# Kernel optimization log

Hardware: AMD Instinct MI355X
Metric: run time of the kernel (lower is better)

## Reference

```python
import jax, jax.numpy as jnp
import numpy as np

SIG_T_TRAIN = 0.07
SIG_T_INFER = 0.07
EPS = 1e-12  # torch F.normalize eps


def _l2_normalize(x):
    # matches torch.nn.functional.normalize(x, dim=-1): x / max(||x||_2, eps)
    nrm = jnp.sqrt(jnp.sum(x * x, axis=-1, keepdims=True))
    return x / jnp.maximum(nrm, EPS)


def setup_inputs() -> dict:
    key = jax.random.key(0)
    k1, k2 = jax.random.split(key)
    v_feat = jax.random.normal(k1, (32, 16, 256, 512), dtype=jnp.float32)  # (b,n,t,d)
    t_feat = jax.random.normal(k2, (512, 512), dtype=jnp.float32)          # (c,d)
    return {"v_feat": v_feat, "t_feat": t_feat, "split": 1}


def reference(v_feat, t_feat, split):
    # split: 1 -> 'test' (normalize + sig_T_infer), 0 -> train (sig_T_train)
    if split == 1:
        tau = SIG_T_INFER
        v_feat = _l2_normalize(v_feat)
        t_feat = _l2_normalize(t_feat)
    else:
        tau = SIG_T_TRAIN
    # Original: dist = einsum('bntd,bmcd->bctnm', v, t_repeated)/tau, then mean over m, then n.
    # t_repeated is identical along m (a pure repeat), so mean over m is a no-op, and the
    # mean over n commutes with the linear contraction: reduce over n first, never
    # materializing the (b,c,t,n,m) tensor.
    v_mean = jnp.mean(v_feat, axis=1)  # (b,t,d)
    dist = jnp.einsum('btd,cd->bct', v_mean, t_feat) / tau  # (b,c,t)
    return dist
```

## Files before the change

kernel.cpp:

```cpp
#include <hip/hip_runtime.h>

typedef unsigned short u16;
typedef unsigned int u32;

typedef __bf16 bf16x8 __attribute__((ext_vector_type(8)));
typedef float f32x4 __attribute__((ext_vector_type(4)));

__device__ __forceinline__ u16 f2bf(float f) {
    u32 u = __float_as_uint(f);
    return (u16)((u + 0x7fffu + ((u >> 16) & 1u)) >> 16);
}

__global__ __launch_bounds__(256, 4) void prep_kernel(
    const float* __restrict__ v,
    const float* __restrict__ tf,
    u16* __restrict__ vm,
    u16* __restrict__ tn,
    const int* __restrict__ splitp)
{
    const int tid  = threadIdx.x;
    const int w    = tid >> 6;
    const int lane = tid & 63;
    const int g    = lane >> 4;
    const int l15  = lane & 15;
    const int split = *splitp;
    const int bxx  = blockIdx.x;

    if (bxx >= 8192) {
        const int row = (bxx - 8192) * 16 + w * 4 + g;
        const float* rp = tf + (size_t)row * 512;
        float4 x[8];
#pragma unroll
        for (int i = 0; i < 8; i++)
            x[i] = *reinterpret_cast<const float4*>(rp + i * 64 + l15 * 4);
        float s = 0.f;
#pragma unroll
        for (int i = 0; i < 8; i++)
            s += x[i].x*x[i].x + x[i].y*x[i].y + x[i].z*x[i].z + x[i].w*x[i].w;
#pragma unroll
        for (int off = 1; off < 16; off <<= 1) s += __shfl_xor(s, off, 64);
        float inv = 1.0f;
        if (split == 1) inv = 1.0f / fmaxf(sqrtf(s), 1e-12f);
        u16* orow = tn + (size_t)row * 512;
#pragma unroll
        for (int i = 0; i < 8; i++) {
            uint2 pk;
            pk.x = (u32)f2bf(x[i].x*inv) | ((u32)f2bf(x[i].y*inv) << 16);
            pk.y = (u32)f2bf(x[i].z*inv) | ((u32)f2bf(x[i].w*inv) << 16);
            *reinterpret_cast<uint2*>(orow + i * 64 + l15 * 4) = pk;
        }
        return;
    }

    const int b = bxx >> 8;
    const int t = bxx & 255;
    const int n = w * 4 + g;
    const float* rp = v + (((size_t)(b * 16 + n) * 256) + t) * 512;

    float4 x[8];
#pragma unroll
    for (int i = 0; i < 8; i++)
        x[i] = *reinterpret_cast<const float4*>(rp + i * 64 + l15 * 4);

    float s = 0.f;
#pragma unroll
    for (int i = 0; i < 8; i++)
        s += x[i].x*x[i].x + x[i].y*x[i].y + x[i].z*x[i].z + x[i].w*x[i].w;
#pragma unroll
    for (int off = 1; off < 16; off <<= 1) s += __shfl_xor(s, off, 64);
    float inv = 1.0f;
    if (split == 1) inv = 1.0f / fmaxf(sqrtf(s), 1e-12f);

#pragma unroll
    for (int i = 0; i < 8; i++) {
        x[i].x *= inv; x[i].y *= inv; x[i].z *= inv; x[i].w *= inv;
    }

#pragma unroll
    for (int off = 16; off < 64; off <<= 1)
#pragma unroll
        for (int i = 0; i < 8; i++) {
            x[i].x += __shfl_xor(x[i].x, off, 64);
            x[i].y += __shfl_xor(x[i].y, off, 64);
            x[i].z += __shfl_xor(x[i].z, off, 64);
            x[i].w += __shfl_xor(x[i].w, off, 64);
        }

    __shared__ float lds[4][512];
#pragma unroll
    for (int i = 0; i < 8; i++) {
        if ((i >> 1) == g)
            *reinterpret_cast<float4*>(&lds[w][i * 64 + l15 * 4]) = x[i];
    }
    __syncthreads();

    float2 r; r.x = 0.f; r.y = 0.f;
#pragma unroll
    for (int w2 = 0; w2 < 4; w2++) {
        float2 p = *reinterpret_cast<const float2*>(&lds[w2][tid * 2]);
        r.x += p.x; r.y += p.y;
    }
    r.x *= 0.0625f; r.y *= 0.0625f;
    u32 packed = (u32)f2bf(r.x) | ((u32)f2bf(r.y) << 16);
    reinterpret_cast<u32*>(vm)[((size_t)(b * 256 + t) << 8) + tid] = packed;
}

__global__ __launch_bounds__(256) void gemm_kernel(
    const u16* __restrict__ tn,
    const u16* __restrict__ vm,
    float* __restrict__ out)
{
    const int tid  = threadIdx.x;
    const int lane = tid & 63;
    const int wid  = tid >> 6;
    const int wm   = wid & 1;
    const int wn   = wid >> 1;
    const int quad = lane >> 4;
    const int l15  = lane & 15;

    const int c0 = blockIdx.x * 64 + wm * 32;
    const int t0 = blockIdx.y * 64 + wn * 32;
    const int b  = blockIdx.z;

    const u16* A0 = tn + (size_t)(c0 + l15) * 512 + quad * 8;
    const u16* B0 = vm + (size_t)b * 131072 + (size_t)(t0 + l15) * 512 + quad * 8;

    f32x4 acc[2][2] = {};
#pragma unroll 4
    for (int kk = 0; kk < 512; kk += 32) {
        bf16x8 af[2], bf[2];
#pragma unroll
        for (int i = 0; i < 2; i++)
            af[i] = *reinterpret_cast<const bf16x8*>(A0 + (size_t)i * 16 * 512 + kk);
#pragma unroll
        for (int j = 0; j < 2; j++)
            bf[j] = *reinterpret_cast<const bf16x8*>(B0 + (size_t)j * 16 * 512 + kk);
#pragma unroll
        for (int i = 0; i < 2; i++)
#pragma unroll
            for (int j = 0; j < 2; j++)
                acc[i][j] = __builtin_amdgcn_mfma_f32_16x16x32_bf16(
                    af[i], bf[j], acc[i][j], 0, 0, 0);
    }

    const float sc = 1.0f / 0.07f;
    float* ob = out + (size_t)b * 131072;
#pragma unroll
    for (int i = 0; i < 2; i++)
#pragma unroll
        for (int j = 0; j < 2; j++)
#pragma unroll
            for (int r = 0; r < 4; r++)
                ob[(c0 + i * 16 + quad * 4 + r) * 256 + (t0 + j * 16 + l15)]
                    = acc[i][j][r] * sc;
}

extern "C" void kernel_launch(void* const* d_in, const int* in_sizes, int n_in,
                              void* d_out, int out_size, void* d_ws, size_t ws_size,
                              hipStream_t stream) {
    const float* v_feat = (const float*)d_in[0];
    const float* t_feat = (const float*)d_in[1];
    const int*   splitp = (const int*)d_in[2];
    float* out = (float*)d_out;

    u16* tn = (u16*)d_ws;
    u16* vm = tn + 512 * 512;

    prep_kernel<<<dim3(8192 + 32), dim3(256), 0, stream>>>(v_feat, t_feat, vm, tn, splitp);
    gemm_kernel<<<dim3(8, 4, 32), dim3(256), 0, stream>>>(tn, vm, out);
}
```

Before: 389.4 us.

## Stage GEMM operands through padded LDS tiles with larger 128x64 block tile

The GEMM kernel now cooperatively loads 128x64 A and 64x64 B tiles into padded shared memory per 64-wide K step, and each wave reads its MFMA fragments from LDS instead of straight from global memory. The block tile grows from 64x64 to 128x64, so each wave computes 4x2 MFMA tiles and the grid halves in x. The aim is more operand reuse and fewer redundant global loads. The cost is extra barriers, LDS traffic and fewer blocks. The GEMM is small next to the memory-bound prep kernel, which reads 256MB, so the total effect is likely minor.

```diff
diff --git a/kernel.cpp b/kernel.cpp
--- a/kernel.cpp
+++ b/kernel.cpp
@@ -105,11 +105,12 @@
     reinterpret_cast<u32*>(vm)[((size_t)(b * 256 + t) << 8) + tid] = packed;
 }
 
-__global__ __launch_bounds__(256) void gemm_kernel(
-    const u16* __restrict__ tn,
-    const u16* __restrict__ vm,
-    float* __restrict__ out)
-{
+__global__ __launch_bounds__(256) void gemm_kernel(const u16* __restrict__ tn,
+                                                   const u16* __restrict__ vm,
+                                                   float* __restrict__ out) {
+    const int bx   = blockIdx.x;
+    const int by   = blockIdx.y;
+    const int b    = blockIdx.z;
     const int tid  = threadIdx.x;
     const int lane = tid & 63;
     const int wid  = tid >> 6;
@@ -118,41 +119,65 @@
     const int quad = lane >> 4;
     const int l15  = lane & 15;
 
-    const int c0 = blockIdx.x * 64 + wm * 32;
-    const int t0 = blockIdx.y * 64 + wn * 32;
-    const int b  = blockIdx.z;
+    __shared__ u16 At[128 * 72];
+    __shared__ u16 Bt[64 * 72];
 
-    const u16* A0 = tn + (size_t)(c0 + l15) * 512 + quad * 8;
-    const u16* B0 = vm + (size_t)b * 131072 + (size_t)(t0 + l15) * 512 + quad * 8;
+    const int c0 = bx * 128, t0 = by * 64;
+    f32x4 acc[4][2] = {};
 
-    f32x4 acc[2][2] = {};
-#pragma unroll 4
-    for (int kk = 0; kk < 512; kk += 32) {
-        bf16x8 af[2], bf[2];
+    const int lrow = tid >> 3;
+    const int lcol = (tid & 7) * 8;
+
+    const uint4* gA = reinterpret_cast<const uint4*>(tn);
+    const uint4* gB = reinterpret_cast<const uint4*>(vm) + (size_t)b * 256 * 64;
+
+    for (int k0 = 0; k0 < 512; k0 += 64) {
 #pragma unroll
-        for (int i = 0; i < 2; i++)
-            af[i] = *reinterpret_cast<const bf16x8*>(A0 + (size_t)i * 16 * 512 + kk);
+        for (int it = 0; it < 4; it++) {
+            int row = lrow + it * 32;
+            uint4 av = gA[(c0 + row) * 64 + (k0 >> 3) + (tid & 7)];
+            *reinterpret_cast<uint4*>(&At[row * 72 + lcol]) = av;
+        }
 #pragma unroll
-        for (int j = 0; j < 2; j++)
-            bf[j] = *reinterpret_cast<const bf16x8*>(B0 + (size_t)j * 16 * 512 + kk);
+        for (int it = 0; it < 2; it++) {
+            int row = lrow + it * 32;
+            uint4 bv = gB[(t0 + row) * 64 + (k0 >> 3) + (tid & 7)];
+            *reinterpret_cast<uint4*>(&Bt[row * 72 + lcol]) = bv;
+        }
+        __syncthreads();
 #pragma unroll
-        for (int i = 0; i < 2; i++)
+        for (int kk = 0; kk < 64; kk += 32) {
+            bf16x8 af[4], bfr[2];
+#pragma unroll
+            for (int i = 0; i < 4; i++)
+                af[i] = *reinterpret_cast<const bf16x8*>(
+                    &At[(wm * 64 + i * 16 + l15) * 72 + kk + quad * 8]);
 #pragma unroll
             for (int j = 0; j < 2; j++)
-                acc[i][j] = __builtin_amdgcn_mfma_f32_16x16x32_bf16(
-                    af[i], bf[j], acc[i][j], 0, 0, 0);
+                bfr[j] = *reinterpret_cast<const bf16x8*>(
+                    &Bt[(wn * 32 + j * 16 + l15) * 72 + kk + quad * 8]);
+#pragma unroll
+            for (int i = 0; i < 4; i++)
+#pragma unroll
+                for (int j = 0; j < 2; j++)
+                    acc[i][j] = __builtin_amdgcn_mfma_f32_16x16x32_bf16(
+                        af[i], bfr[j], acc[i][j], 0, 0, 0);
+        }
+        __syncthreads();
     }
 
-    const float sc = 1.0f / 0.07f;
+    const float s = 1.0f / 0.07f;
     float* ob = out + (size_t)b * 131072;
 #pragma unroll
-    for (int i = 0; i < 2; i++)
+    for (int i = 0; i < 4; i++)
 #pragma unroll
         for (int j = 0; j < 2; j++)
 #pragma unroll
-            for (int r = 0; r < 4; r++)
-                ob[(c0 + i * 16 + quad * 4 + r) * 256 + (t0 + j * 16 + l15)]
-                    = acc[i][j][r] * sc;
+            for (int r = 0; r < 4; r++) {
+                int c = c0 + wm * 64 + i * 16 + quad * 4 + r;
+                int t = t0 + wn * 32 + j * 16 + l15;
+                ob[c * 256 + t] = acc[i][j][r] * s;
+            }
 }
 
 extern "C" void kernel_launch(void* const* d_in, const int* in_sizes, int n_in,
@@ -167,5 +192,5 @@
     u16* vm = tn + 512 * 512;
 
     prep_kernel<<<dim3(8192 + 32), dim3(256), 0, stream>>>(v_feat, t_feat, vm, tn, splitp);
-    gemm_kernel<<<dim3(8, 4, 32), dim3(256), 0, stream>>>(tn, vm, out);
+    gemm_kernel<<<dim3(4, 4, 32), dim3(256), 0, stream>>>(tn, vm, out);
 }
```

Result: faster. 369.8 us (-5.0%).
